# Optimization experiments

Hardware: AMD Instinct MI355X
Metric: run time of the kernel (lower is better)

Reference implementation:

```python
import jax, jax.numpy as jnp
import numpy as np

B, DIM, H, W = 64, 256, 5, 5


def setup_inputs() -> dict:
    key = jax.random.key(0)
    k1 = jax.random.fold_in(key, 1)
    feat_map = jax.random.normal(k1, (B, DIM, H, W), dtype=jnp.float32)
    # nn.Parameter init: log(1 / (2 * h * w)) * ones(1, 1)
    temperature = jnp.full((1, 1), float(np.log(1.0 / (2 * H * W))), dtype=jnp.float32)
    return {"feat_map": feat_map, "temperature": temperature}


def reference(feat_map, temperature):
    # comp_relation with lego=False, normalize_bdc=True, out_map=False, no_diag=False
    b, d, h, w = feat_map.shape
    f = feat_map.reshape(b, d, h * w)                     # [B, d, hw]
    # pairwise channel correlation: sum_p |f_i + f_j| - |f_i - f_j|
    s_plus = jnp.sum(jnp.abs(f[:, :, None, :] + f[:, None, :, :]), axis=-1)   # [B, d, d]
    s_minus = jnp.sum(jnp.abs(f[:, :, None, :] - f[:, None, :, :]), axis=-1)  # [B, d, d]
    out = (s_plus - s_minus) * 0.5 * jnp.exp(temperature[0, 0])
    # centering: out - (1/d) out @ ones - (1/d) ones @ out
    row_mean = jnp.sum(out, axis=2, keepdims=True) / d    # (out @ I_M) / d, broadcast over cols
    col_mean = jnp.sum(out, axis=1, keepdims=True) / d    # (I_M @ out) / d, broadcast over rows
    out = out - row_mean - col_mean
    # Triuvec (including diagonal), row-major order as in torch nonzero of triu mask
    iu, ju = jnp.triu_indices(d)
    return out[:, iu, ju]                                 # [B, d*(d+1)/2]
```

## Files before the change

### kernel.cpp

```cpp
#include <hip/hip_runtime.h>
#include <math.h>

#define NB   64
#define D    256
#define HW   25
#define TRI  32896
#define TS   64
#define PSTR 68

__device__ __forceinline__ void tile_bands(int t, int& bi, int& bj) {
    bi = (t < 4) ? 0 : (t < 7) ? 1 : (t < 9) ? 2 : 3;
    const int o4 = (bi == 0) ? 0 : (bi == 1) ? 4 : (bi == 2) ? 7 : 9;
    bj = bi + (t - o4);
}

__global__ __launch_bounds__(256) void tile_kernel(const float* __restrict__ feat,
                                                   float* __restrict__ rsp,
                                                   float* __restrict__ out) {
    __shared__ __align__(16) float as[HW * PSTR];
    __shared__ __align__(16) float bs[HW * PSTR];
    __shared__ float red[2][TS][17];

    const int tid = threadIdx.x;
    const int blk = blockIdx.x;
    const int b   = blk / 10;
    const int t   = blk - b * 10;
    int bi, bj; tile_bands(t, bi, bj);
    const int ibase = bi * TS, jbase = bj * TS;
    const bool diag = (bi == bj);

    const float* fb = feat + (size_t)b * D * HW;

    for (int idx = tid; idx < TS * HW; idx += 256) {
        int r = idx / HW;
        int p = idx - r * HW;
        as[p * PSTR + r] = fb[(ibase + r) * HW + p];
        bs[p * PSTR + r] = fb[(jbase + r) * HW + p];
    }
    __syncthreads();

    const int tx = tid & 15;
    const int ty = tid >> 4;

    float acc[4][4] = {{0.f}};
    for (int p = 0; p < HW; ++p) {
        float4 av = *reinterpret_cast<const float4*>(&as[p * PSTR + ty * 4]);
        float4 bv = *reinterpret_cast<const float4*>(&bs[p * PSTR + tx * 4]);
        float a4[4] = {av.x, av.y, av.z, av.w};
        float b4[4] = {bv.x, bv.y, bv.z, bv.w};
#pragma unroll
        for (int r = 0; r < 4; ++r)
#pragma unroll
            for (int q = 0; q < 4; ++q)
                acc[r][q] += fabsf(a4[r] + b4[q]) - fabsf(a4[r] - b4[q]);
    }

    float* ob = out + (size_t)b * TRI;
#pragma unroll
    for (int r = 0; r < 4; ++r) {
        const int i = ibase + ty * 4 + r;
        const int rowoff = (i * (513 - i)) >> 1;
#pragma unroll
        for (int q = 0; q < 4; ++q) {
            const int j = jbase + tx * 4 + q;
            if (!diag || j >= i) ob[rowoff + (j - i)] = acc[r][q];
        }
    }

    float pi[4], pj[4];
#pragma unroll
    for (int r = 0; r < 4; ++r) pi[r] = acc[r][0] + acc[r][1] + acc[r][2] + acc[r][3];
#pragma unroll
    for (int q = 0; q < 4; ++q) pj[q] = acc[0][q] + acc[1][q] + acc[2][q] + acc[3][q];
#pragma unroll
    for (int r = 0; r < 4; ++r) red[0][ty * 4 + r][tx] = pi[r];
#pragma unroll
    for (int q = 0; q < 4; ++q) red[1][tx * 4 + q][ty] = pj[q];
    __syncthreads();

    if (tid < TS) {
        float si = 0.f;
#pragma unroll
        for (int x = 0; x < 16; ++x) si += red[0][tid][x];
        rsp[((b * 4 + bi) * 4 + (bj - bi)) * TS + tid] = si;
        if (!diag) {
            float sj = 0.f;
#pragma unroll
            for (int x = 0; x < 16; ++x) sj += red[1][tid][x];
            rsp[((b * 4 + bj) * 4 + (4 - bj + bi)) * TS + tid] = sj;
        }
    }
}

__global__ __launch_bounds__(256) void center_kernel(const float* __restrict__ temp,
                                                     const float* __restrict__ rsp,
                                                     float* __restrict__ out) {
    __shared__ float rsum[2][TS];

    const int tid = threadIdx.x;
    const int blk = blockIdx.x;
    const int b   = blk / 10;
    const int t   = blk - b * 10;
    int bi, bj; tile_bands(t, bi, bj);
    const int ibase = bi * TS, jbase = bj * TS;
    const bool diag = (bi == bj);

    if (tid < TS) {
        float s = 0.f;
#pragma unroll
        for (int sl = 0; sl < 4; ++sl) s += rsp[((b * 4 + bi) * 4 + sl) * TS + tid];
        rsum[0][tid] = s;
    } else if (tid < 2 * TS) {
        const int il = tid - TS;
        float s = 0.f;
#pragma unroll
        for (int sl = 0; sl < 4; ++sl) s += rsp[((b * 4 + bj) * 4 + sl) * TS + il];
        rsum[1][il] = s;
    }
    __syncthreads();

    const int tx = tid & 15;
    const int ty = tid >> 4;
    const float sc = 0.5f * expf(temp[0]);
    float* ob = out + (size_t)b * TRI;

#pragma unroll
    for (int r = 0; r < 4; ++r) {
        const int i = ibase + ty * 4 + r;
        const int rowoff = (i * (513 - i)) >> 1;
        const float ri = rsum[0][ty * 4 + r];
#pragma unroll
        for (int q = 0; q < 4; ++q) {
            const int j = jbase + tx * 4 + q;
            if (!diag || j >= i) {
                float* p = &ob[rowoff + (j - i)];
                const float e = *p;
                *p = sc * (e - (ri + rsum[1][tx * 4 + q]) * (1.0f / 256.0f));
            }
        }
    }
}

extern "C" void kernel_launch(void* const* d_in, const int* in_sizes, int n_in,
                              void* d_out, int out_size, void* d_ws, size_t ws_size,
                              hipStream_t stream) {
    const float* feat = (const float*)d_in[0];
    const float* temp = (const float*)d_in[1];
    float* out = (float*)d_out;
    float* rsp = (float*)d_ws;

    tile_kernel<<<NB * 10, 256, 0, stream>>>(feat, rsp, out);
    center_kernel<<<NB * 10, 256, 0, stream>>>(temp, rsp, out);
}
```

Baseline: 28.57 us.

## Split each 64x64 tile into two 64x32 halves with 128-thread blocks

Each upper-triangular 64x64 tile is split into two 64x32 column halves, so there are twice as many blocks with half the threads each (1280 blocks of 128 threads in total). The partial row-sum workspace is reorganised into eight slots per band to hold the half-tile partials, and the center kernel sums a variable number of slots. The p loop is also fully unrolled and the shared-memory loads are made coalesced by p-major indexing. The intent is better occupancy and wave balance across the GPU's compute units, at the cost of loading the A band twice per tile.

```diff
diff --git a/kernel.cpp b/kernel.cpp
--- a/kernel.cpp
+++ b/kernel.cpp
@@ -5,8 +5,8 @@
 #define D    256
 #define HW   25
 #define TRI  32896
-#define TS   64
-#define PSTR 68
+#define ASTR 68
+#define BSTR 36
 
 __device__ __forceinline__ void tile_bands(int t, int& bi, int& bj) {
     bi = (t < 4) ? 0 : (t < 7) ? 1 : (t < 9) ? 2 : 3;
@@ -14,38 +14,49 @@
     bj = bi + (t - o4);
 }
 
-__global__ __launch_bounds__(256) void tile_kernel(const float* __restrict__ feat,
+__device__ __forceinline__ void decode_blk(int blk, int& b, int& bi, int& bj, int& h) {
+    b = blk / 20;
+    const int rem = blk - b * 20;
+    const int t = rem >> 1;
+    h = rem & 1;
+    tile_bands(t, bi, bj);
+}
+
+__global__ __launch_bounds__(128) void tile_kernel(const float* __restrict__ feat,
                                                    float* __restrict__ rsp,
                                                    float* __restrict__ out) {
-    __shared__ __align__(16) float as[HW * PSTR];
-    __shared__ __align__(16) float bs[HW * PSTR];
-    __shared__ float red[2][TS][17];
+    __shared__ __align__(16) float as[HW * ASTR];
+    __shared__ __align__(16) float bs[HW * BSTR];
+    __shared__ float red0[64][9];
+    __shared__ float red1[32][17];
 
     const int tid = threadIdx.x;
-    const int blk = blockIdx.x;
-    const int b   = blk / 10;
-    const int t   = blk - b * 10;
-    int bi, bj; tile_bands(t, bi, bj);
-    const int ibase = bi * TS, jbase = bj * TS;
+    int b, bi, bj, h;
+    decode_blk(blockIdx.x, b, bi, bj, h);
+    const int ibase = bi * 64;
+    const int jbase = bj * 64 + h * 32;
     const bool diag = (bi == bj);
 
     const float* fb = feat + (size_t)b * D * HW;
 
-    for (int idx = tid; idx < TS * HW; idx += 256) {
-        int r = idx / HW;
-        int p = idx - r * HW;
-        as[p * PSTR + r] = fb[(ibase + r) * HW + p];
-        bs[p * PSTR + r] = fb[(jbase + r) * HW + p];
+    for (int idx = tid; idx < HW * 64; idx += 128) {
+        const int p = idx >> 6, r = idx & 63;
+        as[p * ASTR + r] = fb[(ibase + r) * HW + p];
+    }
+    for (int idx = tid; idx < HW * 32; idx += 128) {
+        const int p = idx >> 5, c = idx & 31;
+        bs[p * BSTR + c] = fb[(jbase + c) * HW + p];
     }
     __syncthreads();
 
-    const int tx = tid & 15;
-    const int ty = tid >> 4;
+    const int tx = tid & 7;
+    const int ty = tid >> 3;
 
     float acc[4][4] = {{0.f}};
+#pragma unroll
     for (int p = 0; p < HW; ++p) {
-        float4 av = *reinterpret_cast<const float4*>(&as[p * PSTR + ty * 4]);
-        float4 bv = *reinterpret_cast<const float4*>(&bs[p * PSTR + tx * 4]);
+        float4 av = *reinterpret_cast<const float4*>(&as[p * ASTR + ty * 4]);
+        float4 bv = *reinterpret_cast<const float4*>(&bs[p * BSTR + tx * 4]);
         float a4[4] = {av.x, av.y, av.z, av.w};
         float b4[4] = {bv.x, bv.y, bv.z, bv.w};
 #pragma unroll
@@ -73,54 +84,56 @@
 #pragma unroll
     for (int q = 0; q < 4; ++q) pj[q] = acc[0][q] + acc[1][q] + acc[2][q] + acc[3][q];
 #pragma unroll
-    for (int r = 0; r < 4; ++r) red[0][ty * 4 + r][tx] = pi[r];
+    for (int r = 0; r < 4; ++r) red0[ty * 4 + r][tx] = pi[r];
 #pragma unroll
-    for (int q = 0; q < 4; ++q) red[1][tx * 4 + q][ty] = pj[q];
+    for (int q = 0; q < 4; ++q) red1[tx * 4 + q][ty] = pj[q];
     __syncthreads();
 
-    if (tid < TS) {
-        float si = 0.f;
+    if (tid < 64) {
+        float s = 0.f;
 #pragma unroll
-        for (int x = 0; x < 16; ++x) si += red[0][tid][x];
-        rsp[((b * 4 + bi) * 4 + (bj - bi)) * TS + tid] = si;
-        if (!diag) {
-            float sj = 0.f;
+        for (int x = 0; x < 8; ++x) s += red0[tid][x];
+        rsp[(((b * 4 + bi) * 8) + (bj - bi) * 2 + h) * 64 + tid] = s;
+    } else if (tid < 96 && !diag) {
+        const int c = tid - 64;
+        float s = 0.f;
 #pragma unroll
-            for (int x = 0; x < 16; ++x) sj += red[1][tid][x];
-            rsp[((b * 4 + bj) * 4 + (4 - bj + bi)) * TS + tid] = sj;
-        }
+        for (int x = 0; x < 16; ++x) s += red1[c][x];
+        rsp[(((b * 4 + bj) * 8) + (4 - bj) * 2 + bi) * 64 + h * 32 + c] = s;
     }
 }
 
-__global__ __launch_bounds__(256) void center_kernel(const float* __restrict__ temp,
+__global__ __launch_bounds__(128) void center_kernel(const float* __restrict__ temp,
                                                      const float* __restrict__ rsp,
                                                      float* __restrict__ out) {
-    __shared__ float rsum[2][TS];
+    __shared__ float rsum0[64];
+    __shared__ float rsum1[32];
 
     const int tid = threadIdx.x;
-    const int blk = blockIdx.x;
-    const int b   = blk / 10;
-    const int t   = blk - b * 10;
-    int bi, bj; tile_bands(t, bi, bj);
-    const int ibase = bi * TS, jbase = bj * TS;
+    int b, bi, bj, h;
+    decode_blk(blockIdx.x, b, bi, bj, h);
+    const int ibase = bi * 64;
+    const int jbase = bj * 64 + h * 32;
     const bool diag = (bi == bj);
 
-    if (tid < TS) {
+    if (tid < 64) {
+        const int ns = 8 - bi;
         float s = 0.f;
-#pragma unroll
-        for (int sl = 0; sl < 4; ++sl) s += rsp[((b * 4 + bi) * 4 + sl) * TS + tid];
-        rsum[0][tid] = s;
-    } else if (tid < 2 * TS) {
-        const int il = tid - TS;
+        for (int sl = 0; sl < ns; ++sl)
+            s += rsp[((b * 4 + bi) * 8 + sl) * 64 + tid];
+        rsum0[tid] = s;
+    } else if (tid < 96) {
+        const int c = tid - 64;
+        const int ns = 8 - bj;
         float s = 0.f;
-#pragma unroll
-        for (int sl = 0; sl < 4; ++sl) s += rsp[((b * 4 + bj) * 4 + sl) * TS + il];
-        rsum[1][il] = s;
+        for (int sl = 0; sl < ns; ++sl)
+            s += rsp[((b * 4 + bj) * 8 + sl) * 64 + h * 32 + c];
+        rsum1[c] = s;
     }
     __syncthreads();
 
-    const int tx = tid & 15;
-    const int ty = tid >> 4;
+    const int tx = tid & 7;
+    const int ty = tid >> 3;
     const float sc = 0.5f * expf(temp[0]);
     float* ob = out + (size_t)b * TRI;
 
@@ -128,14 +141,14 @@
     for (int r = 0; r < 4; ++r) {
         const int i = ibase + ty * 4 + r;
         const int rowoff = (i * (513 - i)) >> 1;
-        const float ri = rsum[0][ty * 4 + r];
+        const float ri = rsum0[ty * 4 + r];
 #pragma unroll
         for (int q = 0; q < 4; ++q) {
             const int j = jbase + tx * 4 + q;
             if (!diag || j >= i) {
                 float* p = &ob[rowoff + (j - i)];
                 const float e = *p;
-                *p = sc * (e - (ri + rsum[1][tx * 4 + q]) * (1.0f / 256.0f));
+                *p = sc * (e - (ri + rsum1[tx * 4 + q]) * (1.0f / 256.0f));
             }
         }
     }
@@ -149,6 +162,6 @@
     float* out = (float*)d_out;
     float* rsp = (float*)d_ws;
 
-    tile_kernel<<<NB * 10, 256, 0, stream>>>(feat, rsp, out);
-    center_kernel<<<NB * 10, 256, 0, stream>>>(temp, rsp, out);
+    tile_kernel<<<NB * 20, 128, 0, stream>>>(feat, rsp, out);
+    center_kernel<<<NB * 20, 128, 0, stream>>>(temp, rsp, out);
 }
```

After: 35.39 us. 1.24x slower.
